# Optimization experiments

Hardware: AMD Instinct MI355X
Metric: run time of the kernel (lower is better)

Reference implementation:

```python
import jax, jax.numpy as jnp
import numpy as np

ALPHA = 1.0
EPS = 1e-6


def setup_inputs() -> dict:
    key = jax.random.key(0)
    ks = jax.random.split(key, 6)
    B, d_lat, hidden, n_genes = 256, 32, 512, 4000
    z = jax.random.normal(ks[0], (B, d_lat), dtype=jnp.float32)
    W1 = jax.random.normal(ks[1], (d_lat, hidden), dtype=jnp.float32) / np.sqrt(d_lat)
    b1 = jnp.zeros((hidden,), dtype=jnp.float32)
    W2 = jax.random.normal(ks[2], (hidden, n_genes), dtype=jnp.float32) / np.sqrt(hidden)
    b2 = jnp.zeros((n_genes,), dtype=jnp.float32)
    log_theta = 0.5 * jax.random.normal(ks[3], (n_genes,), dtype=jnp.float32)
    return {"z": z, "W1": W1, "b1": b1, "W2": W2, "b2": b2, "log_theta": log_theta}


def _decode_mu(z_vec, W1, b1, W2, b2):
    # NB decoder mean for a single latent vector; lib_dummy == 1 so no scaling.
    h = jax.nn.relu(z_vec @ W1 + b1)            # [hidden]
    return jax.nn.softplus(h @ W2 + b2)          # [n_genes]


def reference(z, W1, b1, W2, b2, log_theta):
    d_lat = z.shape[1]
    theta = jnp.exp(log_theta)                   # [G], per-gene dispersion

    f = lambda zv: _decode_mu(zv, W1, b1, W2, b2)

    mu = jax.vmap(f)(z)                          # [B, G]
    J = jax.vmap(jax.jacfwd(f))(z)               # [B, G, d_lat]

    # weights computed under no_grad in the original
    mu_ng = jax.lax.stop_gradient(mu)
    weights = theta / (mu_ng * (mu_ng + theta) + EPS)   # [B, G]

    # Gram[b, i, j] = sum_g J[b,g,i] * w[b,g] * J[b,g,j]  (== U @ U.T with U = sqrt(w)*J^T)
    Gram = jnp.einsum('bgi,bg,bgj->bij', J, weights, J)  # [B, d_lat, d_lat]

    eye = jnp.eye(d_lat, dtype=z.dtype)
    losses = jnp.sum((Gram - ALPHA * eye) ** 2, axis=(1, 2))  # [B]
    return jnp.mean(losses)
```

## Files before the change

### kernel.cpp

```cpp
#include <hip/hip_runtime.h>

typedef __bf16 bf16x8 __attribute__((ext_vector_type(8)));
typedef float f32x4 __attribute__((ext_vector_type(4)));
typedef unsigned short u16x8 __attribute__((ext_vector_type(8)));

typedef const void __attribute__((address_space(1)))* gas_ptr;
typedef void __attribute__((address_space(3)))* las_ptr;

#define GLOAD16(gp, lp) __builtin_amdgcn_global_load_lds((gas_ptr)(gp), (las_ptr)(lp), 16, 0, 0)

__device__ __forceinline__ unsigned short f2bf(float f) {
  unsigned int u = __float_as_uint(f);
  u += 0x7FFF + ((u >> 16) & 1);
  return (unsigned short)(u >> 16);
}
__device__ __forceinline__ float bf2f(unsigned short u) {
  return __uint_as_float(((unsigned int)u) << 16);
}

__global__ __launch_bounds__(256) void k_prep2(const float* __restrict__ W2,
                                               unsigned short* __restrict__ W2T,
                                               const float* __restrict__ z,
                                               const float* __restrict__ W1,
                                               const float* __restrict__ b1,
                                               unsigned short* __restrict__ Hb,
                                               unsigned short* __restrict__ Astack) {
  __shared__ float tile[64][65];
  const int t = threadIdx.x;
  if (blockIdx.y < 8) {
    const int gt = blockIdx.x;
    const int jt = blockIdx.y;
    const int c = t & 63, r4 = t >> 6;
#pragma unroll
    for (int r = 0; r < 16; ++r) {
      int jj = r * 4 + r4;
      int g = gt * 64 + c;
      tile[jj][c] = (g < 4000) ? W2[(size_t)(jt * 64 + jj) * 4000 + g] : 0.f;
    }
    __syncthreads();
#pragma unroll
    for (int r = 0; r < 16; ++r) {
      int gg = r * 4 + r4;
      W2T[(size_t)(gt * 64 + gg) * 512 + jt * 64 + c] = f2bf(tile[c][gg]);
    }
  } else {
    float* zs = &tile[0][0];
    unsigned char* mk = (unsigned char*)&tile[2][0];
    for (int s = 0; s < 4; ++s) {
      int b = blockIdx.x * 4 + s;
      __syncthreads();
      if (t < 32) zs[t] = z[b * 32 + t];
      __syncthreads();
#pragma unroll
      for (int jj = 0; jj < 2; ++jj) {
        int j = t + jj * 256;
        float a = b1[j];
#pragma unroll
        for (int i = 0; i < 32; ++i) a = fmaf(zs[i], W1[i * 512 + j], a);
        bool m = a > 0.f;
        mk[j] = m ? 1 : 0;
        Hb[b * 512 + j] = m ? f2bf(a) : (unsigned short)0;
      }
      __syncthreads();
#pragma unroll
      for (int k = 0; k < 8; ++k) {
        int c8 = t + k * 256;
        int row = c8 >> 6;
        int k8 = (c8 & 63) * 8;
        unsigned long long m8 = *(const unsigned long long*)(mk + k8);
        const float* w = W1 + row * 512 + k8;
        u16x8 out;
#pragma unroll
        for (int e = 0; e < 8; ++e)
          out[e] = ((m8 >> (e * 8)) & 0xffULL) ? f2bf(w[e]) : (unsigned short)0;
        *(u16x8*)(Astack + ((size_t)(b * 32 + row)) * 512 + k8) = out;
      }
    }
  }
}

__global__ __launch_bounds__(256) void k_s3(const unsigned short* __restrict__ Hb,
                                            const unsigned short* __restrict__ W2T,
                                            const float* __restrict__ b2,
                                            const float* __restrict__ log_theta,
                                            float* __restrict__ Cw) {
  __shared__ __align__(16) char smem[24576];
  char* Abuf = smem;
  char* Bbuf = smem + 8192;

  const int bm = blockIdx.x;
  const int g0 = blockIdx.y * 64;
  const int t = threadIdx.x;
  const int lane = t & 63;
  const int wave = t >> 6;
  const int l8 = lane >> 3;
  const int kxor = (((lane & 7) ^ l8) << 3);
  const int c16 = lane & 15;
  const int lg = lane >> 4;

  f32x4 acc[2];
  acc[0] = (f32x4){0.f, 0.f, 0.f, 0.f};
  acc[1] = (f32x4){0.f, 0.f, 0.f, 0.f};

#define STAGE_S3(buf, kt)                                                             \
  do {                                                                                \
    GLOAD16(Hb + (size_t)(bm * 32 + wave * 8 + l8) * 512 + (kt) * 64 + kxor,          \
            Abuf + (buf) * 4096 + wave * 1024);                                       \
    _Pragma("unroll") for (int qq = 0; qq < 2; ++qq) {                                \
      int q = wave * 2 + qq;                                                          \
      GLOAD16(W2T + (size_t)(g0 + q * 8 + l8) * 512 + (kt) * 64 + kxor,               \
              Bbuf + (buf) * 8192 + q * 1024);                                        \
    }                                                                                 \
  } while (0)

  STAGE_S3(0, 0);
  __syncthreads();

  for (int kt = 0; kt < 8; ++kt) {
    int cur = kt & 1;
    if (kt < 7) STAGE_S3(cur ^ 1, kt + 1);
    const char* Ab = Abuf + cur * 4096;
    const char* Bb = Bbuf + cur * 8192;
#pragma unroll
    for (int ks = 0; ks < 2; ++ks) {
      int kb = ks * 64 + lg * 16;
      bf16x8 av[2], bv;
#pragma unroll
      for (int mt = 0; mt < 2; ++mt) {
        int row = mt * 16 + c16;
        av[mt] = *(const bf16x8*)(Ab + (row >> 3) * 1024 + (row & 7) * 128 + (kb ^ ((row & 7) << 4)));
      }
      {
        int row = wave * 16 + c16;
        bv = *(const bf16x8*)(Bb + (row >> 3) * 1024 + (row & 7) * 128 + (kb ^ ((row & 7) << 4)));
      }
#pragma unroll
      for (int mt = 0; mt < 2; ++mt)
        acc[mt] = __builtin_amdgcn_mfma_f32_16x16x32_bf16(av[mt], bv, acc[mt], 0, 0, 0);
    }
    __syncthreads();
  }

  {
    int g = g0 + wave * 16 + c16;
    if (g < 4000) {
      float bb = b2[g];
      float theta = expf(log_theta[g]);
#pragma unroll
      for (int mt = 0; mt < 2; ++mt)
#pragma unroll
        for (int r = 0; r < 4; ++r) {
          int sample = bm * 32 + mt * 16 + lg * 4 + r;
          float s = acc[mt][r] + bb;
          float sig = 1.f / (1.f + expf(-s));
          float mu = (s > 20.f) ? s : log1pf(expf(s));
          float w = theta / (mu * (mu + theta) + 1e-6f);
          Cw[(size_t)sample * 4096 + g] = w * sig * sig;
        }
    } else {
#pragma unroll
      for (int mt = 0; mt < 2; ++mt)
#pragma unroll
        for (int r = 0; r < 4; ++r) {
          int sample = bm * 32 + mt * 16 + lg * 4 + r;
          Cw[(size_t)sample * 4096 + g] = 0.f;
        }
    }
  }
}

__global__ __launch_bounds__(512, 2) void k_gemm(const unsigned short* __restrict__ Astack,
                                                 const unsigned short* __restrict__ W2T,
                                                 const float* __restrict__ Cw,
                                                 float* __restrict__ Gram) {
  extern __shared__ __align__(16) char smem[];
  char* AbufB = smem;
  char* BbufB = smem + 65536;

  const int bm = blockIdx.x;
  const int g0 = blockIdx.y * 256;
  const int t = threadIdx.x;
  const int lane = t & 63;
  const int wave = t >> 6;
  const int wr = wave >> 2;
  const int wc = wave & 3;
  const int kxor = (((t & 7) ^ ((t >> 3) & 7)) << 3);
  const int c16 = lane & 15;
  const int lg = lane >> 4;

  f32x4 acc[8][4];
#pragma unroll
  for (int mt = 0; mt < 8; ++mt)
#pragma unroll
    for (int nt = 0; nt < 4; ++nt) acc[mt][nt] = (f32x4){0.f, 0.f, 0.f, 0.f};

  const unsigned short* Aptr = Astack + (size_t)bm * 256 * 512;
  const unsigned short* Bptr = W2T + (size_t)g0 * 512;
  const int trow = t >> 3;

#define STAGE_BIG(buf, kt)                                                            \
  do {                                                                                \
    _Pragma("unroll") for (int q = 0; q < 4; ++q)                                     \
      GLOAD16(Aptr + (size_t)(q * 64 + trow) * 512 + (kt) * 64 + kxor,                \
              AbufB + (buf) * 32768 + q * 8192 + wave * 1024);                        \
    _Pragma("unroll") for (int q = 0; q < 4; ++q)                                     \
      GLOAD16(Bptr + (size_t)(q * 64 + trow) * 512 + (kt) * 64 + kxor,                \
              BbufB + (buf) * 32768 + q * 8192 + wave * 1024);                        \
  } while (0)

  STAGE_BIG(0, 0);
  __syncthreads();

  for (int kt = 0; kt < 8; ++kt) {
    int cur = kt & 1;
    if (kt < 7) STAGE_BIG(cur ^ 1, kt + 1);
    const char* Ab = AbufB + cur * 32768;
    const char* Bb = BbufB + cur * 32768;
#pragma unroll
    for (int ks = 0; ks < 2; ++ks) {
      int kb = ks * 64 + lg * 16;
      bf16x8 av[8], bv[4];
#pragma unroll
      for (int mt = 0; mt < 8; ++mt) {
        int row = wr * 128 + mt * 16 + c16;
        av[mt] = *(const bf16x8*)(Ab + row * 128 + (kb ^ ((row & 7) << 4)));
      }
#pragma unroll
      for (int nt = 0; nt < 4; ++nt) {
        int row = wc * 64 + nt * 16 + c16;
        bv[nt] = *(const bf16x8*)(Bb + row * 128 + (kb ^ ((row & 7) << 4)));
      }
#pragma unroll
      for (int mt = 0; mt < 8; ++mt)
#pragma unroll
        for (int nt = 0; nt < 4; ++nt)
          acc[mt][nt] = __builtin_amdgcn_mfma_f32_16x16x32_bf16(av[mt], bv[nt], acc[mt][nt], 0, 0, 0);
    }
    __syncthreads();
  }

  float* c_lds = (float*)(smem + 131072);

#pragma unroll
  for (int mt = 0; mt < 8; ++mt)
#pragma unroll
    for (int nt = 0; nt < 4; ++nt)
#pragma unroll
      for (int r = 0; r < 4; ++r) {
        int row = wr * 128 + mt * 16 + lg * 4 + r;
        int col = wc * 64 + nt * 16 + c16;
        *(unsigned short*)(smem + row * 512 + ((col * 2) ^ ((row & 7) << 4))) = f2bf(acc[mt][nt][r]);
      }
#pragma unroll
  for (int k = 0; k < 4; ++k) {
    int e = t + k * 512;
    c_lds[e] = Cw[(size_t)(bm * 8 + (e >> 8)) * 4096 + g0 + (e & 255)];
  }
  __syncthreads();

  {
    const int s = wave;
    f32x4 gacc[2][2];
#pragma unroll
    for (int m2 = 0; m2 < 2; ++m2)
#pragma unroll
      for (int n2 = 0; n2 < 2; ++n2) gacc[m2][n2] = (f32x4){0.f, 0.f, 0.f, 0.f};

#pragma unroll
    for (int ch = 0; ch < 8; ++ch) {
      f32x4 cv0 = *(const f32x4*)(c_lds + s * 256 + ch * 32 + lg * 8);
      f32x4 cv1 = *(const f32x4*)(c_lds + s * 256 + ch * 32 + lg * 8 + 4);
      u16x8 raw[2];
      bf16x8 ap[2], bp[2];
#pragma unroll
      for (int m2 = 0; m2 < 2; ++m2) {
        int row = s * 32 + m2 * 16 + c16;
        raw[m2] = *(const u16x8*)(smem + row * 512 + ((ch * 64 + lg * 16) ^ ((row & 7) << 4)));
        u16x8 sc;
#pragma unroll
        for (int e = 0; e < 4; ++e) sc[e] = f2bf(bf2f(raw[m2][e]) * cv0[e]);
#pragma unroll
        for (int e = 0; e < 4; ++e) sc[4 + e] = f2bf(bf2f(raw[m2][4 + e]) * cv1[e]);
        ap[m2] = __builtin_bit_cast(bf16x8, sc);
        bp[m2] = __builtin_bit_cast(bf16x8, raw[m2]);
      }
#pragma unroll
      for (int m2 = 0; m2 < 2; ++m2)
#pragma unroll
        for (int n2 = 0; n2 < 2; ++n2)
          gacc[m2][n2] = __builtin_amdgcn_mfma_f32_16x16x32_bf16(ap[m2], bp[n2], gacc[m2][n2], 0, 0, 0);
    }

#pragma unroll
    for (int m2 = 0; m2 < 2; ++m2)
#pragma unroll
      for (int n2 = 0; n2 < 2; ++n2)
#pragma unroll
        for (int r = 0; r < 4; ++r) {
          int i = m2 * 16 + lg * 4 + r;
          int j = n2 * 16 + c16;
          atomicAdd(Gram + (size_t)(bm * 8 + s) * 1024 + i * 32 + j, gacc[m2][n2][r]);
        }
  }
}

__global__ __launch_bounds__(256) void k_loss(const float* __restrict__ Gram,
                                              float* __restrict__ out) {
  __shared__ float red[4];
  const int b = blockIdx.x, t = threadIdx.x;
  float local = 0.f;
#pragma unroll
  for (int k = 0; k < 4; ++k) {
    int e = t + k * 256;
    float d = Gram[(size_t)b * 1024 + e] - (((e >> 5) == (e & 31)) ? 1.f : 0.f);
    local += d * d;
  }
#pragma unroll
  for (int off = 32; off > 0; off >>= 1) local += __shfl_down(local, off);
  if ((t & 63) == 0) red[t >> 6] = local;
  __syncthreads();
  if (t == 0) {
    float s = red[0] + red[1] + red[2] + red[3];
    atomicAdd(out, s * (1.f / 256.f));
  }
}

extern "C" void kernel_launch(void* const* d_in, const int* in_sizes, int n_in,
                              void* d_out, int out_size, void* d_ws, size_t ws_size,
                              hipStream_t stream) {
  const float* z = (const float*)d_in[0];
  const float* W1 = (const float*)d_in[1];
  const float* b1 = (const float*)d_in[2];
  const float* W2 = (const float*)d_in[3];
  const float* b2 = (const float*)d_in[4];
  const float* lt = (const float*)d_in[5];

  char* ws = (char*)d_ws;
  unsigned short* W2T = (unsigned short*)ws;
  unsigned short* Astack = (unsigned short*)(ws + 4194304);
  unsigned short* Hb = (unsigned short*)(ws + 12582912);
  float* Cw = (float*)(ws + 12976128);
  float* Gram = (float*)(ws + 17170432);

  hipMemsetAsync(Gram, 0, 256 * 1024 * 4, stream);
  hipMemsetAsync(d_out, 0, 4, stream);

  static const int kGemmLds = 131072 + 8192;
  hipFuncSetAttribute((const void*)k_gemm, hipFuncAttributeMaxDynamicSharedMemorySize, kGemmLds);

  k_prep2<<<dim3(64, 9), 256, 0, stream>>>(W2, W2T, z, W1, b1, Hb, Astack);
  k_s3<<<dim3(8, 64), 256, 0, stream>>>(Hb, W2T, b2, lt, Cw);
  k_gemm<<<dim3(32, 16), 512, kGemmLds, stream>>>(Astack, W2T, Cw, Gram);
  k_loss<<<256, 256, 0, stream>>>(Gram, (float*)d_out);
}
```

Baseline: 166.8 us.

## Pipeline GEMM main loop with half-tile prefetch and split prep kernel

Restructures the k_gemm main loop so that each K-step issues its global-to-LDS loads in two halves interleaved with MFMA clusters. It uses explicit vmcnt waits, raw s_barrier, sched_barrier and setprio in place of full __syncthreads, so that loads overlap compute. It also splits the combined prep kernel into a separate W2 transpose kernel and a per-sample mask/Astack kernel with 256 blocks, which exposes more parallelism in the mask preparation. The manual waitcnt/barrier scheduling is fragile and adds one extra kernel launch.

```diff
diff --git a/kernel.cpp b/kernel.cpp
--- a/kernel.cpp
+++ b/kernel.cpp
@@ -18,64 +18,60 @@
   return __uint_as_float(((unsigned int)u) << 16);
 }
 
-__global__ __launch_bounds__(256) void k_prep2(const float* __restrict__ W2,
-                                               unsigned short* __restrict__ W2T,
-                                               const float* __restrict__ z,
-                                               const float* __restrict__ W1,
-                                               const float* __restrict__ b1,
-                                               unsigned short* __restrict__ Hb,
-                                               unsigned short* __restrict__ Astack) {
+__global__ __launch_bounds__(256) void k_w2t(const float* __restrict__ W2,
+                                             unsigned short* __restrict__ W2T) {
   __shared__ float tile[64][65];
+  const int gt = blockIdx.x;
+  const int jt = blockIdx.y;
   const int t = threadIdx.x;
-  if (blockIdx.y < 8) {
-    const int gt = blockIdx.x;
-    const int jt = blockIdx.y;
-    const int c = t & 63, r4 = t >> 6;
-#pragma unroll
-    for (int r = 0; r < 16; ++r) {
-      int jj = r * 4 + r4;
-      int g = gt * 64 + c;
-      tile[jj][c] = (g < 4000) ? W2[(size_t)(jt * 64 + jj) * 4000 + g] : 0.f;
-    }
-    __syncthreads();
-#pragma unroll
-    for (int r = 0; r < 16; ++r) {
-      int gg = r * 4 + r4;
-      W2T[(size_t)(gt * 64 + gg) * 512 + jt * 64 + c] = f2bf(tile[c][gg]);
-    }
-  } else {
-    float* zs = &tile[0][0];
-    unsigned char* mk = (unsigned char*)&tile[2][0];
-    for (int s = 0; s < 4; ++s) {
-      int b = blockIdx.x * 4 + s;
-      __syncthreads();
-      if (t < 32) zs[t] = z[b * 32 + t];
-      __syncthreads();
-#pragma unroll
-      for (int jj = 0; jj < 2; ++jj) {
-        int j = t + jj * 256;
-        float a = b1[j];
-#pragma unroll
-        for (int i = 0; i < 32; ++i) a = fmaf(zs[i], W1[i * 512 + j], a);
-        bool m = a > 0.f;
-        mk[j] = m ? 1 : 0;
-        Hb[b * 512 + j] = m ? f2bf(a) : (unsigned short)0;
-      }
-      __syncthreads();
-#pragma unroll
-      for (int k = 0; k < 8; ++k) {
-        int c8 = t + k * 256;
-        int row = c8 >> 6;
-        int k8 = (c8 & 63) * 8;
-        unsigned long long m8 = *(const unsigned long long*)(mk + k8);
-        const float* w = W1 + row * 512 + k8;
-        u16x8 out;
-#pragma unroll
-        for (int e = 0; e < 8; ++e)
-          out[e] = ((m8 >> (e * 8)) & 0xffULL) ? f2bf(w[e]) : (unsigned short)0;
-        *(u16x8*)(Astack + ((size_t)(b * 32 + row)) * 512 + k8) = out;
-      }
-    }
+  const int c = t & 63, r4 = t >> 6;
+#pragma unroll
+  for (int r = 0; r < 16; ++r) {
+    int jj = r * 4 + r4;
+    int g = gt * 64 + c;
+    tile[jj][c] = (g < 4000) ? W2[(size_t)(jt * 64 + jj) * 4000 + g] : 0.f;
+  }
+  __syncthreads();
+#pragma unroll
+  for (int r = 0; r < 16; ++r) {
+    int gg = r * 4 + r4;
+    W2T[(size_t)(gt * 64 + gg) * 512 + jt * 64 + c] = f2bf(tile[c][gg]);
+  }
+}
+
+__global__ __launch_bounds__(256) void k_maskprep(const float* __restrict__ z,
+                                                  const float* __restrict__ W1,
+                                                  const float* __restrict__ b1,
+                                                  unsigned short* __restrict__ Hb,
+                                                  unsigned short* __restrict__ Astack) {
+  __shared__ float zs[32];
+  __shared__ __align__(8) unsigned char mk[512];
+  const int b = blockIdx.x, t = threadIdx.x;
+  if (t < 32) zs[t] = z[b * 32 + t];
+  __syncthreads();
+#pragma unroll
+  for (int jj = 0; jj < 2; ++jj) {
+    int j = t + jj * 256;
+    float a = b1[j];
+#pragma unroll
+    for (int i = 0; i < 32; ++i) a = fmaf(zs[i], W1[i * 512 + j], a);
+    bool m = a > 0.f;
+    mk[j] = m ? 1 : 0;
+    Hb[b * 512 + j] = m ? f2bf(a) : (unsigned short)0;
+  }
+  __syncthreads();
+#pragma unroll
+  for (int k = 0; k < 8; ++k) {
+    int c8 = t + k * 256;
+    int row = c8 >> 6;
+    int k8 = (c8 & 63) * 8;
+    unsigned long long m8 = *(const unsigned long long*)(mk + k8);
+    const float* w = W1 + row * 512 + k8;
+    u16x8 out;
+#pragma unroll
+    for (int e = 0; e < 8; ++e)
+      out[e] = ((m8 >> (e * 8)) & 0xffULL) ? f2bf(w[e]) : (unsigned short)0;
+    *(u16x8*)(Astack + ((size_t)(b * 32 + row)) * 512 + k8) = out;
   }
 }
 
@@ -174,17 +170,16 @@
                                                  const float* __restrict__ Cw,
                                                  float* __restrict__ Gram) {
   extern __shared__ __align__(16) char smem[];
-  char* AbufB = smem;
-  char* BbufB = smem + 65536;
 
   const int bm = blockIdx.x;
   const int g0 = blockIdx.y * 256;
   const int t = threadIdx.x;
   const int lane = t & 63;
   const int wave = t >> 6;
-  const int wr = wave >> 2;
-  const int wc = wave & 3;
-  const int kxor = (((t & 7) ^ ((t >> 3) & 7)) << 3);
+  const int wm = wave >> 2;
+  const int wn = wave & 3;
+  const int trow = t >> 3;
+  const int kxor = (((t & 7) ^ (trow & 7)) << 3);
   const int c16 = lane & 15;
   const int lg = lane >> 4;
 
@@ -196,48 +191,83 @@
 
   const unsigned short* Aptr = Astack + (size_t)bm * 256 * 512;
   const unsigned short* Bptr = W2T + (size_t)g0 * 512;
-  const int trow = t >> 3;
-
-#define STAGE_BIG(buf, kt)                                                            \
+
+#define SHALF(b, kt, h)                                                               \
   do {                                                                                \
-    _Pragma("unroll") for (int q = 0; q < 4; ++q)                                     \
-      GLOAD16(Aptr + (size_t)(q * 64 + trow) * 512 + (kt) * 64 + kxor,                \
-              AbufB + (buf) * 32768 + q * 8192 + wave * 1024);                        \
-    _Pragma("unroll") for (int q = 0; q < 4; ++q)                                     \
-      GLOAD16(Bptr + (size_t)(q * 64 + trow) * 512 + (kt) * 64 + kxor,                \
-              BbufB + (buf) * 32768 + q * 8192 + wave * 1024);                        \
+    _Pragma("unroll") for (int q = 0; q < 2; ++q) {                                   \
+      int row = (h) * 128 + q * 64 + trow;                                            \
+      GLOAD16(Aptr + (size_t)row * 512 + (kt) * 64 + kxor,                            \
+              smem + (b) * 65536 + row * 128 + (t & 7) * 16);                         \
+      GLOAD16(Bptr + (size_t)row * 512 + (kt) * 64 + kxor,                            \
+              smem + (b) * 65536 + 32768 + row * 128 + (t & 7) * 16);                 \
+    }                                                                                 \
   } while (0)
 
-  STAGE_BIG(0, 0);
-  __syncthreads();
-
-  for (int kt = 0; kt < 8; ++kt) {
-    int cur = kt & 1;
-    if (kt < 7) STAGE_BIG(cur ^ 1, kt + 1);
-    const char* Ab = AbufB + cur * 32768;
-    const char* Bb = BbufB + cur * 32768;
-#pragma unroll
-    for (int ks = 0; ks < 2; ++ks) {
-      int kb = ks * 64 + lg * 16;
-      bf16x8 av[8], bv[4];
-#pragma unroll
-      for (int mt = 0; mt < 8; ++mt) {
-        int row = wr * 128 + mt * 16 + c16;
-        av[mt] = *(const bf16x8*)(Ab + row * 128 + (kb ^ ((row & 7) << 4)));
-      }
-#pragma unroll
-      for (int nt = 0; nt < 4; ++nt) {
-        int row = wc * 64 + nt * 16 + c16;
-        bv[nt] = *(const bf16x8*)(Bb + row * 128 + (kb ^ ((row & 7) << 4)));
-      }
-#pragma unroll
-      for (int mt = 0; mt < 8; ++mt)
-#pragma unroll
-        for (int nt = 0; nt < 4; ++nt)
-          acc[mt][nt] = __builtin_amdgcn_mfma_f32_16x16x32_bf16(av[mt], bv[nt], acc[mt][nt], 0, 0, 0);
+#define LOAD_BV(cur)                                                                  \
+  _Pragma("unroll") for (int nt = 0; nt < 4; ++nt)                                    \
+  _Pragma("unroll") for (int ks = 0; ks < 2; ++ks) {                                  \
+    int row = wn * 64 + nt * 16 + c16;                                                \
+    bv[nt][ks] = *(const bf16x8*)(smem + (cur) * 65536 + 32768 + row * 128 +          \
+                                  ((ks * 64 + lg * 16) ^ ((row & 7) << 4)));          \
+  }
+
+#define LOAD_AV(cur, mh)                                                              \
+  _Pragma("unroll") for (int mi = 0; mi < 4; ++mi)                                    \
+  _Pragma("unroll") for (int ks = 0; ks < 2; ++ks) {                                  \
+    int row = wm * 128 + ((mh) * 4 + mi) * 16 + c16;                                  \
+    av[mi][ks] = *(const bf16x8*)(smem + (cur) * 65536 + row * 128 +                  \
+                                  ((ks * 64 + lg * 16) ^ ((row & 7) << 4)));          \
+  }
+
+#define MFMA_CLUSTER(mh)                                                              \
+  __builtin_amdgcn_s_setprio(1);                                                      \
+  _Pragma("unroll") for (int ks = 0; ks < 2; ++ks)                                    \
+  _Pragma("unroll") for (int mi = 0; mi < 4; ++mi)                                    \
+  _Pragma("unroll") for (int nt = 0; nt < 4; ++nt)                                    \
+    acc[(mh) * 4 + mi][nt] =                                                          \
+        __builtin_amdgcn_mfma_f32_16x16x32_bf16(av[mi][ks], bv[nt][ks],               \
+                                                acc[(mh) * 4 + mi][nt], 0, 0, 0);     \
+  __builtin_amdgcn_s_setprio(0);
+
+  SHALF(0, 0, 0);
+  SHALF(0, 0, 1);
+  SHALF(1, 1, 0);
+
+#pragma unroll
+  for (int kt = 0; kt < 7; ++kt) {
+    const int cur = kt & 1;
+    const int nxt = cur ^ 1;
+    asm volatile("s_waitcnt vmcnt(4)" ::: "memory");
+    __builtin_amdgcn_s_barrier();
+    __builtin_amdgcn_sched_barrier(0);
+    {
+      bf16x8 bv[4][2], av[4][2];
+      LOAD_BV(cur)
+      LOAD_AV(cur, 0)
+      MFMA_CLUSTER(0)
+      SHALF(nxt, kt + 1, 1);
+      LOAD_AV(cur, 1)
+      MFMA_CLUSTER(1)
     }
-    __syncthreads();
-  }
+    __builtin_amdgcn_sched_barrier(0);
+    __builtin_amdgcn_s_barrier();
+    __builtin_amdgcn_sched_barrier(0);
+    if (kt < 6) SHALF(cur, kt + 2, 0);
+  }
+  asm volatile("s_waitcnt vmcnt(0)" ::: "memory");
+  __builtin_amdgcn_s_barrier();
+  __builtin_amdgcn_sched_barrier(0);
+  {
+    bf16x8 bv[4][2], av[4][2];
+    LOAD_BV(1)
+    LOAD_AV(1, 0)
+    MFMA_CLUSTER(0)
+    LOAD_AV(1, 1)
+    MFMA_CLUSTER(1)
+  }
+  __builtin_amdgcn_sched_barrier(0);
+  __builtin_amdgcn_s_barrier();
+  __builtin_amdgcn_sched_barrier(0);
 
   float* c_lds = (float*)(smem + 131072);
 
@@ -247,8 +277,8 @@
     for (int nt = 0; nt < 4; ++nt)
 #pragma unroll
       for (int r = 0; r < 4; ++r) {
-        int row = wr * 128 + mt * 16 + lg * 4 + r;
-        int col = wc * 64 + nt * 16 + c16;
+        int row = wm * 128 + mt * 16 + lg * 4 + r;
+        int col = wn * 64 + nt * 16 + c16;
         *(unsigned short*)(smem + row * 512 + ((col * 2) ^ ((row & 7) << 4))) = f2bf(acc[mt][nt][r]);
       }
 #pragma unroll
@@ -348,7 +378,8 @@
   static const int kGemmLds = 131072 + 8192;
   hipFuncSetAttribute((const void*)k_gemm, hipFuncAttributeMaxDynamicSharedMemorySize, kGemmLds);
 
-  k_prep2<<<dim3(64, 9), 256, 0, stream>>>(W2, W2T, z, W1, b1, Hb, Astack);
+  k_w2t<<<dim3(64, 8), 256, 0, stream>>>(W2, W2T);
+  k_maskprep<<<256, 256, 0, stream>>>(z, W1, b1, Hb, Astack);
   k_s3<<<dim3(8, 64), 256, 0, stream>>>(Hb, W2T, b2, lt, Cw);
   k_gemm<<<dim3(32, 16), 512, kGemmLds, stream>>>(Astack, W2T, Cw, Gram);
   k_loss<<<256, 256, 0, stream>>>(Gram, (float*)d_out);
```

New measurement: 147.5 us. 11.6% less time.

## Fuse decoder-mean GEMM and weight computation into the Gram GEMM kernel

Applied to the files above, without the earlier changes.

Removes the separate k_s3 kernel and the Cw buffer. Each k_gemm block now loads its 8 samples' hidden activations into LDS and computes the pre-activation with extra MFMAs on the already-staged W2T tiles, then derives the per-gene weights in the epilogue. The prep kernel is split into a W2 transpose kernel and a per-sample mask kernel with more parallelism. This trades a launch and a global round trip for extra LDS and MFMA work done by only half the waves.

```diff
diff --git a/kernel.cpp b/kernel.cpp
--- a/kernel.cpp
+++ b/kernel.cpp
@@ -18,173 +18,80 @@
   return __uint_as_float(((unsigned int)u) << 16);
 }
 
-__global__ __launch_bounds__(256) void k_prep2(const float* __restrict__ W2,
-                                               unsigned short* __restrict__ W2T,
-                                               const float* __restrict__ z,
-                                               const float* __restrict__ W1,
-                                               const float* __restrict__ b1,
-                                               unsigned short* __restrict__ Hb,
-                                               unsigned short* __restrict__ Astack) {
+__global__ __launch_bounds__(256) void k_w2t(const float* __restrict__ W2,
+                                             unsigned short* __restrict__ W2T) {
   __shared__ float tile[64][65];
+  const int gt = blockIdx.x;
+  const int jt = blockIdx.y;
   const int t = threadIdx.x;
-  if (blockIdx.y < 8) {
-    const int gt = blockIdx.x;
-    const int jt = blockIdx.y;
-    const int c = t & 63, r4 = t >> 6;
-#pragma unroll
-    for (int r = 0; r < 16; ++r) {
-      int jj = r * 4 + r4;
-      int g = gt * 64 + c;
-      tile[jj][c] = (g < 4000) ? W2[(size_t)(jt * 64 + jj) * 4000 + g] : 0.f;
-    }
-    __syncthreads();
-#pragma unroll
-    for (int r = 0; r < 16; ++r) {
-      int gg = r * 4 + r4;
-      W2T[(size_t)(gt * 64 + gg) * 512 + jt * 64 + c] = f2bf(tile[c][gg]);
-    }
-  } else {
-    float* zs = &tile[0][0];
-    unsigned char* mk = (unsigned char*)&tile[2][0];
-    for (int s = 0; s < 4; ++s) {
-      int b = blockIdx.x * 4 + s;
-      __syncthreads();
-      if (t < 32) zs[t] = z[b * 32 + t];
-      __syncthreads();
-#pragma unroll
-      for (int jj = 0; jj < 2; ++jj) {
-        int j = t + jj * 256;
-        float a = b1[j];
-#pragma unroll
-        for (int i = 0; i < 32; ++i) a = fmaf(zs[i], W1[i * 512 + j], a);
-        bool m = a > 0.f;
-        mk[j] = m ? 1 : 0;
-        Hb[b * 512 + j] = m ? f2bf(a) : (unsigned short)0;
-      }
-      __syncthreads();
-#pragma unroll
-      for (int k = 0; k < 8; ++k) {
-        int c8 = t + k * 256;
-        int row = c8 >> 6;
-        int k8 = (c8 & 63) * 8;
-        unsigned long long m8 = *(const unsigned long long*)(mk + k8);
-        const float* w = W1 + row * 512 + k8;
-        u16x8 out;
-#pragma unroll
-        for (int e = 0; e < 8; ++e)
-          out[e] = ((m8 >> (e * 8)) & 0xffULL) ? f2bf(w[e]) : (unsigned short)0;
-        *(u16x8*)(Astack + ((size_t)(b * 32 + row)) * 512 + k8) = out;
-      }
-    }
-  }
-}
-
-__global__ __launch_bounds__(256) void k_s3(const unsigned short* __restrict__ Hb,
-                                            const unsigned short* __restrict__ W2T,
-                                            const float* __restrict__ b2,
-                                            const float* __restrict__ log_theta,
-                                            float* __restrict__ Cw) {
-  __shared__ __align__(16) char smem[24576];
-  char* Abuf = smem;
-  char* Bbuf = smem + 8192;
-
-  const int bm = blockIdx.x;
-  const int g0 = blockIdx.y * 64;
-  const int t = threadIdx.x;
-  const int lane = t & 63;
-  const int wave = t >> 6;
-  const int l8 = lane >> 3;
-  const int kxor = (((lane & 7) ^ l8) << 3);
-  const int c16 = lane & 15;
-  const int lg = lane >> 4;
-
-  f32x4 acc[2];
-  acc[0] = (f32x4){0.f, 0.f, 0.f, 0.f};
-  acc[1] = (f32x4){0.f, 0.f, 0.f, 0.f};
-
-#define STAGE_S3(buf, kt)                                                             \
-  do {                                                                                \
-    GLOAD16(Hb + (size_t)(bm * 32 + wave * 8 + l8) * 512 + (kt) * 64 + kxor,          \
-            Abuf + (buf) * 4096 + wave * 1024);                                       \
-    _Pragma("unroll") for (int qq = 0; qq < 2; ++qq) {                                \
-      int q = wave * 2 + qq;                                                          \
-      GLOAD16(W2T + (size_t)(g0 + q * 8 + l8) * 512 + (kt) * 64 + kxor,               \
-              Bbuf + (buf) * 8192 + q * 1024);                                        \
-    }                                                                                 \
-  } while (0)
-
-  STAGE_S3(0, 0);
-  __syncthreads();
-
-  for (int kt = 0; kt < 8; ++kt) {
-    int cur = kt & 1;
-    if (kt < 7) STAGE_S3(cur ^ 1, kt + 1);
-    const char* Ab = Abuf + cur * 4096;
-    const char* Bb = Bbuf + cur * 8192;
-#pragma unroll
-    for (int ks = 0; ks < 2; ++ks) {
-      int kb = ks * 64 + lg * 16;
-      bf16x8 av[2], bv;
-#pragma unroll
-      for (int mt = 0; mt < 2; ++mt) {
-        int row = mt * 16 + c16;
-        av[mt] = *(const bf16x8*)(Ab + (row >> 3) * 1024 + (row & 7) * 128 + (kb ^ ((row & 7) << 4)));
-      }
-      {
-        int row = wave * 16 + c16;
-        bv = *(const bf16x8*)(Bb + (row >> 3) * 1024 + (row & 7) * 128 + (kb ^ ((row & 7) << 4)));
-      }
-#pragma unroll
-      for (int mt = 0; mt < 2; ++mt)
-        acc[mt] = __builtin_amdgcn_mfma_f32_16x16x32_bf16(av[mt], bv, acc[mt], 0, 0, 0);
-    }
-    __syncthreads();
-  }
-
-  {
-    int g = g0 + wave * 16 + c16;
-    if (g < 4000) {
-      float bb = b2[g];
-      float theta = expf(log_theta[g]);
-#pragma unroll
-      for (int mt = 0; mt < 2; ++mt)
-#pragma unroll
-        for (int r = 0; r < 4; ++r) {
-          int sample = bm * 32 + mt * 16 + lg * 4 + r;
-          float s = acc[mt][r] + bb;
-          float sig = 1.f / (1.f + expf(-s));
-          float mu = (s > 20.f) ? s : log1pf(expf(s));
-          float w = theta / (mu * (mu + theta) + 1e-6f);
-          Cw[(size_t)sample * 4096 + g] = w * sig * sig;
-        }
-    } else {
-#pragma unroll
-      for (int mt = 0; mt < 2; ++mt)
-#pragma unroll
-        for (int r = 0; r < 4; ++r) {
-          int sample = bm * 32 + mt * 16 + lg * 4 + r;
-          Cw[(size_t)sample * 4096 + g] = 0.f;
-        }
-    }
+  const int c = t & 63, r4 = t >> 6;
+#pragma unroll
+  for (int r = 0; r < 16; ++r) {
+    int jj = r * 4 + r4;
+    int g = gt * 64 + c;
+    tile[jj][c] = (g < 4000) ? W2[(size_t)(jt * 64 + jj) * 4000 + g] : 0.f;
+  }
+  __syncthreads();
+#pragma unroll
+  for (int r = 0; r < 16; ++r) {
+    int gg = r * 4 + r4;
+    W2T[(size_t)(gt * 64 + gg) * 512 + jt * 64 + c] = f2bf(tile[c][gg]);
+  }
+}
+
+__global__ __launch_bounds__(256) void k_maskprep(const float* __restrict__ z,
+                                                  const float* __restrict__ W1,
+                                                  const float* __restrict__ b1,
+                                                  unsigned short* __restrict__ Hb,
+                                                  unsigned short* __restrict__ Astack) {
+  __shared__ float zs[32];
+  __shared__ __align__(8) unsigned char mk[512];
+  const int b = blockIdx.x, t = threadIdx.x;
+  if (t < 32) zs[t] = z[b * 32 + t];
+  __syncthreads();
+#pragma unroll
+  for (int jj = 0; jj < 2; ++jj) {
+    int j = t + jj * 256;
+    float a = b1[j];
+#pragma unroll
+    for (int i = 0; i < 32; ++i) a = fmaf(zs[i], W1[i * 512 + j], a);
+    bool m = a > 0.f;
+    mk[j] = m ? 1 : 0;
+    Hb[b * 512 + j] = m ? f2bf(a) : (unsigned short)0;
+  }
+  __syncthreads();
+#pragma unroll
+  for (int k = 0; k < 8; ++k) {
+    int c8 = t + k * 256;
+    int row = c8 >> 6;
+    int k8 = (c8 & 63) * 8;
+    unsigned long long m8 = *(const unsigned long long*)(mk + k8);
+    const float* w = W1 + row * 512 + k8;
+    u16x8 out;
+#pragma unroll
+    for (int e = 0; e < 8; ++e)
+      out[e] = ((m8 >> (e * 8)) & 0xffULL) ? f2bf(w[e]) : (unsigned short)0;
+    *(u16x8*)(Astack + ((size_t)(b * 32 + row)) * 512 + k8) = out;
   }
 }
 
 __global__ __launch_bounds__(512, 2) void k_gemm(const unsigned short* __restrict__ Astack,
                                                  const unsigned short* __restrict__ W2T,
-                                                 const float* __restrict__ Cw,
+                                                 const unsigned short* __restrict__ Hb,
+                                                 const float* __restrict__ b2,
+                                                 const float* __restrict__ log_theta,
                                                  float* __restrict__ Gram) {
   extern __shared__ __align__(16) char smem[];
-  char* AbufB = smem;
-  char* BbufB = smem + 65536;
 
   const int bm = blockIdx.x;
   const int g0 = blockIdx.y * 256;
   const int t = threadIdx.x;
   const int lane = t & 63;
   const int wave = t >> 6;
-  const int wr = wave >> 2;
-  const int wc = wave & 3;
-  const int kxor = (((t & 7) ^ ((t >> 3) & 7)) << 3);
+  const int wm = wave >> 2;
+  const int wn = wave & 3;
+  const int trow = t >> 3;
+  const int kxor = (((t & 7) ^ (trow & 7)) << 3);
   const int c16 = lane & 15;
   const int lg = lane >> 4;
 
@@ -193,41 +100,59 @@
   for (int mt = 0; mt < 8; ++mt)
 #pragma unroll
     for (int nt = 0; nt < 4; ++nt) acc[mt][nt] = (f32x4){0.f, 0.f, 0.f, 0.f};
+  f32x4 sacc[4];
+#pragma unroll
+  for (int nt = 0; nt < 4; ++nt) sacc[nt] = (f32x4){0.f, 0.f, 0.f, 0.f};
 
   const unsigned short* Aptr = Astack + (size_t)bm * 256 * 512;
   const unsigned short* Bptr = W2T + (size_t)g0 * 512;
-  const int trow = t >> 3;
+  char* H_lds = smem + 139264;
 
 #define STAGE_BIG(buf, kt)                                                            \
   do {                                                                                \
     _Pragma("unroll") for (int q = 0; q < 4; ++q)                                     \
       GLOAD16(Aptr + (size_t)(q * 64 + trow) * 512 + (kt) * 64 + kxor,                \
-              AbufB + (buf) * 32768 + q * 8192 + wave * 1024);                        \
+              smem + (buf) * 65536 + q * 8192 + wave * 1024);                         \
     _Pragma("unroll") for (int q = 0; q < 4; ++q)                                     \
       GLOAD16(Bptr + (size_t)(q * 64 + trow) * 512 + (kt) * 64 + kxor,                \
-              BbufB + (buf) * 32768 + q * 8192 + wave * 1024);                        \
+              smem + (buf) * 65536 + 32768 + q * 8192 + wave * 1024);                 \
   } while (0)
 
   STAGE_BIG(0, 0);
+
+#pragma unroll
+  for (int i = 0; i < 2; ++i) {
+    int o = t * 2 + i;
+    int row = o >> 6;
+    int col8 = (o & 63) * 8;
+    u16x8 v;
+    if (row < 8) {
+      v = *(const u16x8*)(Hb + (size_t)(bm * 8 + row) * 512 + col8);
+    } else {
+#pragma unroll
+      for (int e = 0; e < 8; ++e) v[e] = 0;
+    }
+    *(u16x8*)(H_lds + row * 1024 + ((col8 * 2) ^ ((row & 7) << 4))) = v;
+  }
   __syncthreads();
 
   for (int kt = 0; kt < 8; ++kt) {
     int cur = kt & 1;
     if (kt < 7) STAGE_BIG(cur ^ 1, kt + 1);
-    const char* Ab = AbufB + cur * 32768;
-    const char* Bb = BbufB + cur * 32768;
+    const char* Ab = smem + cur * 65536;
+    const char* Bb = smem + cur * 65536 + 32768;
 #pragma unroll
     for (int ks = 0; ks < 2; ++ks) {
       int kb = ks * 64 + lg * 16;
       bf16x8 av[8], bv[4];
 #pragma unroll
       for (int mt = 0; mt < 8; ++mt) {
-        int row = wr * 128 + mt * 16 + c16;
+        int row = wm * 128 + mt * 16 + c16;
         av[mt] = *(const bf16x8*)(Ab + row * 128 + (kb ^ ((row & 7) << 4)));
       }
 #pragma unroll
       for (int nt = 0; nt < 4; ++nt) {
-        int row = wc * 64 + nt * 16 + c16;
+        int row = wn * 64 + nt * 16 + c16;
         bv[nt] = *(const bf16x8*)(Bb + row * 128 + (kb ^ ((row & 7) << 4)));
       }
 #pragma unroll
@@ -235,6 +160,13 @@
 #pragma unroll
         for (int nt = 0; nt < 4; ++nt)
           acc[mt][nt] = __builtin_amdgcn_mfma_f32_16x16x32_bf16(av[mt], bv[nt], acc[mt][nt], 0, 0, 0);
+      if (wm == 0) {
+        bf16x8 hv = *(const bf16x8*)(H_lds + c16 * 1024 +
+                                     (((kt * 64 + ks * 32 + lg * 8) * 2) ^ ((c16 & 7) << 4)));
+#pragma unroll
+        for (int nt = 0; nt < 4; ++nt)
+          sacc[nt] = __builtin_amdgcn_mfma_f32_16x16x32_bf16(hv, bv[nt], sacc[nt], 0, 0, 0);
+      }
     }
     __syncthreads();
   }
@@ -247,14 +179,30 @@
     for (int nt = 0; nt < 4; ++nt)
 #pragma unroll
       for (int r = 0; r < 4; ++r) {
-        int row = wr * 128 + mt * 16 + lg * 4 + r;
-        int col = wc * 64 + nt * 16 + c16;
+        int row = wm * 128 + mt * 16 + lg * 4 + r;
+        int col = wn * 64 + nt * 16 + c16;
         *(unsigned short*)(smem + row * 512 + ((col * 2) ^ ((row & 7) << 4))) = f2bf(acc[mt][nt][r]);
       }
-#pragma unroll
-  for (int k = 0; k < 4; ++k) {
-    int e = t + k * 512;
-    c_lds[e] = Cw[(size_t)(bm * 8 + (e >> 8)) * 4096 + g0 + (e & 255)];
+
+  if (wm == 0) {
+#pragma unroll
+    for (int nt = 0; nt < 4; ++nt) {
+      int col = wn * 64 + nt * 16 + c16;
+      int gg = g0 + col;
+      float bb = (gg < 4000) ? b2[gg] : 0.f;
+      float th = (gg < 4000) ? expf(log_theta[gg]) : 1.f;
+#pragma unroll
+      for (int r = 0; r < 4; ++r) {
+        int srow = lg * 4 + r;
+        if (srow < 8) {
+          float s = sacc[nt][r] + bb;
+          float sig = 1.f / (1.f + expf(-s));
+          float mu = (s > 20.f) ? s : log1pf(expf(s));
+          float w = th / (mu * (mu + th) + 1e-6f);
+          c_lds[srow * 256 + col] = (gg < 4000) ? (w * sig * sig) : 0.f;
+        }
+      }
+    }
   }
   __syncthreads();
 
@@ -339,17 +287,16 @@
   unsigned short* W2T = (unsigned short*)ws;
   unsigned short* Astack = (unsigned short*)(ws + 4194304);
   unsigned short* Hb = (unsigned short*)(ws + 12582912);
-  float* Cw = (float*)(ws + 12976128);
   float* Gram = (float*)(ws + 17170432);
 
   hipMemsetAsync(Gram, 0, 256 * 1024 * 4, stream);
   hipMemsetAsync(d_out, 0, 4, stream);
 
-  static const int kGemmLds = 131072 + 8192;
+  static const int kGemmLds = 139264 + 16384;
   hipFuncSetAttribute((const void*)k_gemm, hipFuncAttributeMaxDynamicSharedMemorySize, kGemmLds);
 
-  k_prep2<<<dim3(64, 9), 256, 0, stream>>>(W2, W2T, z, W1, b1, Hb, Astack);
-  k_s3<<<dim3(8, 64), 256, 0, stream>>>(Hb, W2T, b2, lt, Cw);
-  k_gemm<<<dim3(32, 16), 512, kGemmLds, stream>>>(Astack, W2T, Cw, Gram);
+  k_w2t<<<dim3(64, 8), 256, 0, stream>>>(W2, W2T);
+  k_maskprep<<<256, 256, 0, stream>>>(z, W1, b1, Hb, Astack);
+  k_gemm<<<dim3(32, 16), 512, kGemmLds, stream>>>(Astack, W2T, Hb, b2, lt, Gram);
   k_loss<<<256, 256, 0, stream>>>(Gram, (float*)d_out);
 }
```

Measured after the change: 149.6 us. 10.3% less time.
